# Kernel optimization log

Hardware: AMD Instinct MI355X
Metric: run time of the kernel (lower is better)

## Reference

```python
import jax, jax.numpy as jnp
import numpy as np
import math


def setup_inputs() -> dict:
    key = jax.random.key(0)
    k1, k2, k3 = jax.random.split(key, 3)
    B, H, T, D = 4, 16, 4096, 128
    return {
        "q": jax.random.normal(k1, (B, H, T, D), dtype=jnp.float32),
        "k": jax.random.normal(k2, (B, H, T, D), dtype=jnp.float32),
        "v": jax.random.normal(k3, (B, H, T, D), dtype=jnp.float32),
        "BS": 32,
    }


def _compress(x, block_size):
    # blockwise mean-pool along T: [B,H,T,D] -> [B,H,C,D], C = ceil(T/BS)
    B, H, T, D = x.shape
    C = math.ceil(T / block_size)
    pad = C * block_size - T
    if pad:
        x = jnp.pad(x, ((0, 0), (0, 0), (0, pad), (0, 0)))
    return x.reshape(B, H, C, block_size, D).mean(axis=3)


def reference(q, k, v, BS):
    dk = k.shape[-1]
    k_cmp = _compress(k, BS)  # [B,H,C,D]
    v_cmp = _compress(v, BS)  # [B,H,C,D]
    # scaled dot-product attention over compressed KV
    score = jnp.einsum("bhtd,bhcd->bhtc", q, k_cmp) / math.sqrt(dk)
    score = jax.nn.softmax(score, axis=-1)  # [B,H,T,C]
    out = jnp.einsum("bhtc,bhcd->bhtd", score, v_cmp)  # [B,H,T,D]
    return (out, score)
```

## Files before the change

### kernel.cpp

```cpp
#include <hip/hip_runtime.h>
#include <hip/hip_bf16.h>

typedef __attribute__((ext_vector_type(8))) short short8;
typedef __attribute__((ext_vector_type(4))) float f32x4;

#define B_  4
#define H_  16
#define T_  4096
#define D_  128
#define BS_ 32
#define C_  128
#define BH_ (B_ * H_)

__device__ __forceinline__ int posperm(int x) {
  return (x & ~31) | (((x >> 2) & 3) << 3) | (((x >> 4) & 1) << 2) | (x & 3);
}

__device__ __forceinline__ unsigned short f2bf(float f) {
  __hip_bfloat16 h = __float2bfloat16(f);
  return __builtin_bit_cast(unsigned short, h);
}

__device__ __forceinline__ void gload_lds16(const uint4* g, uint4* l) {
  __builtin_amdgcn_global_load_lds(
      (const __attribute__((address_space(1))) unsigned int*)g,
      (__attribute__((address_space(3))) unsigned int*)l, 16, 0, 0);
}

__global__ __launch_bounds__(256) void compress_kernel(
    const float* __restrict__ k, const float* __restrict__ v,
    unsigned short* __restrict__ kc, unsigned short* __restrict__ vT) {
  int blk = blockIdx.x;
  int bh  = blk >> 4;
  int cg  = blk & 15;
  int cb  = cg * 8 + (threadIdx.x >> 5);
  int l   = threadIdx.x & 31;
  const float* kp = k + ((size_t)bh * T_ + (size_t)cb * BS_) * D_ + 4 * l;
  const float* vp = v + ((size_t)bh * T_ + (size_t)cb * BS_) * D_ + 4 * l;
  float4 ks = {0.f, 0.f, 0.f, 0.f}, vs = {0.f, 0.f, 0.f, 0.f};
#pragma unroll
  for (int j = 0; j < BS_; ++j) {
    float4 a = *(const float4*)(kp + (size_t)j * D_);
    float4 b = *(const float4*)(vp + (size_t)j * D_);
    ks.x += a.x; ks.y += a.y; ks.z += a.z; ks.w += a.w;
    vs.x += b.x; vs.y += b.y; vs.z += b.z; vs.w += b.w;
  }
  const float s  = 1.0f / BS_;
  const float sk = s * 0.08838834764831845f;
  size_t slab = (size_t)bh * (C_ * D_);
  unsigned short kq[4] = {f2bf(ks.x * sk), f2bf(ks.y * sk), f2bf(ks.z * sk), f2bf(ks.w * sk)};
  int p0 = posperm(4 * l) ^ ((cb & 7) << 3);
  *(uint2*)&kc[slab + (size_t)cb * D_ + p0] = *(const uint2*)kq;
  float vv[4] = {vs.x * s, vs.y * s, vs.z * s, vs.w * s};
#pragma unroll
  for (int i = 0; i < 4; ++i) {
    int d = 4 * l + i;
    vT[slab + (size_t)d * C_ + (posperm(cb) ^ ((d & 7) << 3))] = f2bf(vv[i]);
  }
}

__global__ __launch_bounds__(256, 4) void attn_kernel(
    const float* __restrict__ q, const unsigned short* __restrict__ kc,
    const unsigned short* __restrict__ vT, float* __restrict__ out,
    float* __restrict__ score) {
  __shared__ uint4 sbuf[2048];

  int blk    = blockIdx.x;
  int bh     = blk >> 6;
  int tchunk = blk & 63;
  int tid    = threadIdx.x;
  int wave   = tid >> 6;
  int lane   = tid & 63;
  int g      = lane >> 4;
  int lr     = lane & 15;
  int rx     = lr & 7;
  int t0     = tchunk * 64 + wave * 16;

  const uint4* kg = (const uint4*)(kc + (size_t)bh * (C_ * D_));
  const uint4* vg = (const uint4*)(vT + (size_t)bh * (C_ * D_));

  const float* qrow = q + ((size_t)bh * T_ + t0 + lr) * D_;
  float4 qa[4], qb[4];
#pragma unroll
  for (int ks = 0; ks < 4; ++ks) {
    int d0 = 4 * g + 32 * ks;
    qa[ks] = *(const float4*)(qrow + d0);
    qb[ks] = *(const float4*)(qrow + d0 + 16);
  }

#pragma unroll
  for (int it = 0; it < 8; ++it) gload_lds16(&kg[it * 256 + tid], &sbuf[it * 256 + tid]);

  short8 qf[4];
#pragma unroll
  for (int ks = 0; ks < 4; ++ks) {
    short8 f;
    f[0] = (short)f2bf(qa[ks].x); f[1] = (short)f2bf(qa[ks].y);
    f[2] = (short)f2bf(qa[ks].z); f[3] = (short)f2bf(qa[ks].w);
    f[4] = (short)f2bf(qb[ks].x); f[5] = (short)f2bf(qb[ks].y);
    f[6] = (short)f2bf(qb[ks].z); f[7] = (short)f2bf(qb[ks].w);
    qf[ks] = f;
  }
  __syncthreads();

  f32x4 accS[8];
#pragma unroll
  for (int cm = 0; cm < 8; ++cm) accS[cm] = f32x4{0.f, 0.f, 0.f, 0.f};
#pragma unroll
  for (int cm = 0; cm < 8; ++cm) {
    int rbase = (lr + 16 * cm) * 16;
#pragma unroll
    for (int ks = 0; ks < 4; ++ks) {
      uint4 kf = sbuf[rbase + ((4 * ks + g) ^ rx)];
      accS[cm] = __builtin_amdgcn_mfma_f32_16x16x32_bf16(
          __builtin_bit_cast(short8, kf), qf[ks], accS[cm], 0, 0, 0);
    }
  }

  float m = -3.0e38f;
#pragma unroll
  for (int cm = 0; cm < 8; ++cm)
#pragma unroll
    for (int r = 0; r < 4; ++r) m = fmaxf(m, accS[cm][r]);
  m = fmaxf(m, __shfl_xor(m, 16));
  m = fmaxf(m, __shfl_xor(m, 32));

  float sum = 0.f;
#pragma unroll
  for (int cm = 0; cm < 8; ++cm) {
#pragma unroll
    for (int r = 0; r < 4; ++r) {
      float p = __expf(accS[cm][r] - m);
      accS[cm][r] = p;
      sum += p;
    }
  }
  sum += __shfl_xor(sum, 16);
  sum += __shfl_xor(sum, 32);
  float inv = 1.0f / sum;
#pragma unroll
  for (int cm = 0; cm < 8; ++cm)
#pragma unroll
    for (int r = 0; r < 4; ++r) accS[cm][r] *= inv;

  __syncthreads();

#pragma unroll
  for (int it = 0; it < 8; ++it) gload_lds16(&vg[it * 256 + tid], &sbuf[it * 256 + tid]);
  __builtin_amdgcn_sched_barrier(0);

  float* dstS = score + ((size_t)bh * T_ + t0 + lr) * C_;
#pragma unroll
  for (int cm = 0; cm < 8; ++cm) {
    __builtin_nontemporal_store(accS[cm], (f32x4*)&dstS[16 * cm + 4 * g]);
  }
  __builtin_amdgcn_sched_barrier(0);

  short8 pf[4];
#pragma unroll
  for (int ks = 0; ks < 4; ++ks) {
    short8 f;
#pragma unroll
    for (int r = 0; r < 4; ++r) {
      f[r]     = (short)f2bf(accS[2 * ks][r]);
      f[4 + r] = (short)f2bf(accS[2 * ks + 1][r]);
    }
    pf[ks] = f;
  }

  asm volatile("s_waitcnt vmcnt(8)" ::: "memory");
  __builtin_amdgcn_s_barrier();
  __builtin_amdgcn_sched_barrier(0);

  float* dstO = out + ((size_t)bh * T_ + t0 + lr) * D_;
#pragma unroll
  for (int nt = 0; nt < 8; ++nt) {
    f32x4 o = f32x4{0.f, 0.f, 0.f, 0.f};
    int rbase = (lr + 16 * nt) * 16;
#pragma unroll
    for (int ks = 0; ks < 4; ++ks) {
      uint4 vf = sbuf[rbase + ((4 * ks + g) ^ rx)];
      o = __builtin_amdgcn_mfma_f32_16x16x32_bf16(
          __builtin_bit_cast(short8, vf), pf[ks], o, 0, 0, 0);
    }
    __builtin_nontemporal_store(o, (f32x4*)&dstO[16 * nt + 4 * g]);
  }
}

extern "C" void kernel_launch(void* const* d_in, const int* in_sizes, int n_in,
                              void* d_out, int out_size, void* d_ws, size_t ws_size,
                              hipStream_t stream) {
  const float* q = (const float*)d_in[0];
  const float* k = (const float*)d_in[1];
  const float* v = (const float*)d_in[2];
  float* out   = (float*)d_out;
  float* score = out + (size_t)BH_ * T_ * D_;

  unsigned short* kc = (unsigned short*)d_ws;
  unsigned short* vT = kc + (size_t)BH_ * C_ * D_;

  compress_kernel<<<BH_ * 16, 256, 0, stream>>>(k, v, kc, vT);
  attn_kernel<<<BH_ * 64, 256, 0, stream>>>(q, kc, vT, out, score);
}
```

Measured before the change: 138.3 us.

## Stage score and output tiles through LDS for coalesced row-wide global stores

Score and output tiles are now transposed through per-wave LDS staging buffers, so each row is written as a contiguous 256-byte span instead of scattered 16-byte fragments. To make room for this, the V tile is loaded in two halves and the P·V product is split into two passes: the upper half first, then the lower half, with the staging areas reusing the freed LDS regions. The occupancy hint is also raised from 4 to 5 blocks per CU. In exchange the kernel gains extra LDS traffic and block-wide barriers, and the V load is less overlapped with compute.

```diff
diff --git a/kernel.cpp b/kernel.cpp
--- a/kernel.cpp
+++ b/kernel.cpp
@@ -59,7 +59,7 @@
   }
 }
 
-__global__ __launch_bounds__(256, 4) void attn_kernel(
+__global__ __launch_bounds__(256, 5) void attn_kernel(
     const float* __restrict__ q, const unsigned short* __restrict__ kc,
     const unsigned short* __restrict__ vT, float* __restrict__ out,
     float* __restrict__ score) {
@@ -146,15 +146,27 @@
   __syncthreads();
 
 #pragma unroll
-  for (int it = 0; it < 8; ++it) gload_lds16(&vg[it * 256 + tid], &sbuf[it * 256 + tid]);
+  for (int it = 0; it < 4; ++it)
+    gload_lds16(&vg[1024 + it * 256 + tid], &sbuf[1024 + it * 256 + tid]);
   __builtin_amdgcn_sched_barrier(0);
 
-  float* dstS = score + ((size_t)bh * T_ + t0 + lr) * C_;
-#pragma unroll
-  for (int cm = 0; cm < 8; ++cm) {
-    __builtin_nontemporal_store(accS[cm], (f32x4*)&dstS[16 * cm + 4 * g]);
-  }
-  __builtin_amdgcn_sched_barrier(0);
+  float* bw = (float*)sbuf + wave * 1024;
+  float* dstS = score + ((size_t)bh * T_ + t0) * C_;
+#pragma unroll
+  for (int h = 0; h < 2; ++h) {
+#pragma unroll
+    for (int cq = 0; cq < 4; ++cq) {
+      int c4 = (g + 4 * cq) ^ rx;
+      *(f32x4*)&bw[lr * 64 + c4 * 4] = accS[4 * h + cq];
+    }
+#pragma unroll
+    for (int j = 0; j < 4; ++j) {
+      int row = 4 * j + (lane >> 4);
+      int cq2 = lane & 15;
+      f32x4 val = *(const f32x4*)&bw[row * 64 + (cq2 ^ (row & 7)) * 4];
+      *(f32x4*)&dstS[(size_t)row * C_ + 64 * h + cq2 * 4] = val;
+    }
+  }
 
   short8 pf[4];
 #pragma unroll
@@ -167,23 +179,71 @@
     }
     pf[ks] = f;
   }
-
-  asm volatile("s_waitcnt vmcnt(8)" ::: "memory");
+  __builtin_amdgcn_sched_barrier(0);
+  asm volatile("s_waitcnt vmcnt(8) lgkmcnt(0)" ::: "memory");
   __builtin_amdgcn_s_barrier();
   __builtin_amdgcn_sched_barrier(0);
 
-  float* dstO = out + ((size_t)bh * T_ + t0 + lr) * D_;
-#pragma unroll
-  for (int nt = 0; nt < 8; ++nt) {
-    f32x4 o = f32x4{0.f, 0.f, 0.f, 0.f};
-    int rbase = (lr + 16 * nt) * 16;
+#pragma unroll
+  for (int it = 0; it < 4; ++it)
+    gload_lds16(&vg[it * 256 + tid], &sbuf[it * 256 + tid]);
+
+  f32x4 oB[4];
+#pragma unroll
+  for (int ni = 0; ni < 4; ++ni) oB[ni] = f32x4{0.f, 0.f, 0.f, 0.f};
+#pragma unroll
+  for (int ni = 0; ni < 4; ++ni) {
+    int rbase = (lr + 16 * (4 + ni)) * 16;
 #pragma unroll
     for (int ks = 0; ks < 4; ++ks) {
       uint4 vf = sbuf[rbase + ((4 * ks + g) ^ rx)];
-      o = __builtin_amdgcn_mfma_f32_16x16x32_bf16(
-          __builtin_bit_cast(short8, vf), pf[ks], o, 0, 0, 0);
-    }
-    __builtin_nontemporal_store(o, (f32x4*)&dstO[16 * nt + 4 * g]);
+      oB[ni] = __builtin_amdgcn_mfma_f32_16x16x32_bf16(
+          __builtin_bit_cast(short8, vf), pf[ks], oB[ni], 0, 0, 0);
+    }
+  }
+  __syncthreads();
+
+  float* bwB = (float*)(sbuf + 1024) + wave * 1024;
+  float* dstO = out + ((size_t)bh * T_ + t0) * D_;
+#pragma unroll
+  for (int ni = 0; ni < 4; ++ni) {
+    int c4 = (g + 4 * ni) ^ rx;
+    *(f32x4*)&bwB[lr * 64 + c4 * 4] = oB[ni];
+  }
+#pragma unroll
+  for (int j = 0; j < 4; ++j) {
+    int row = 4 * j + (lane >> 4);
+    int cq2 = lane & 15;
+    f32x4 val = *(const f32x4*)&bwB[row * 64 + (cq2 ^ (row & 7)) * 4];
+    *(f32x4*)&dstO[(size_t)row * D_ + 64 + cq2 * 4] = val;
+  }
+
+  f32x4 oA[4];
+#pragma unroll
+  for (int ni = 0; ni < 4; ++ni) oA[ni] = f32x4{0.f, 0.f, 0.f, 0.f};
+#pragma unroll
+  for (int ni = 0; ni < 4; ++ni) {
+    int rbase = (lr + 16 * ni) * 16;
+#pragma unroll
+    for (int ks = 0; ks < 4; ++ks) {
+      uint4 vf = sbuf[rbase + ((4 * ks + g) ^ rx)];
+      oA[ni] = __builtin_amdgcn_mfma_f32_16x16x32_bf16(
+          __builtin_bit_cast(short8, vf), pf[ks], oA[ni], 0, 0, 0);
+    }
+  }
+  __syncthreads();
+
+#pragma unroll
+  for (int ni = 0; ni < 4; ++ni) {
+    int c4 = (g + 4 * ni) ^ rx;
+    *(f32x4*)&bw[lr * 64 + c4 * 4] = oA[ni];
+  }
+#pragma unroll
+  for (int j = 0; j < 4; ++j) {
+    int row = 4 * j + (lane >> 4);
+    int cq2 = lane & 15;
+    f32x4 val = *(const f32x4*)&bw[row * 64 + (cq2 ^ (row & 7)) * 4];
+    *(f32x4*)&dstO[(size_t)row * D_ + cq2 * 4] = val;
   }
 }
 
```

Result: slower. 147.4 us (+6.6%).
